# Kernel optimization log

Hardware: AMD Instinct MI355X
Metric: run time of the kernel (lower is better)

Reference implementation:

```python
import jax, jax.numpy as jnp
import numpy as np

B, S, DQ, DK, H, D = 4, 2048, 1024, 1024, 16, 64


def setup_inputs() -> dict:
    key = jax.random.key(0)
    k1, k2, k3, k4 = jax.random.split(key, 4)
    # xavier_uniform bound for Linear(in, out): sqrt(6/(in+out))
    bq = float(np.sqrt(6.0 / (DQ + H * D)))
    bk = float(np.sqrt(6.0 / (DK + H * D)))
    return {
        "query_input": jax.random.normal(k1, (B, S, DQ), dtype=jnp.float32),
        "key_input": jax.random.normal(k2, (B, S, DK), dtype=jnp.float32),
        "Wq": jax.random.uniform(k3, (H * D, DQ), minval=-bq, maxval=bq, dtype=jnp.float32),
        "bq": jnp.zeros((H * D,), dtype=jnp.float32),
        "Wk": jax.random.uniform(k4, (H * D, DK), minval=-bk, maxval=bk, dtype=jnp.float32),
        "bk": jnp.zeros((H * D,), dtype=jnp.float32),
    }


def reference(query_input, key_input, Wq, bq, Wk, bk):
    scaling = D ** (-0.5)
    # projections: (B, S, H*D) -> (B, S, H, D)
    q = (query_input @ Wq.T + bq).reshape(B, S, H, D) * scaling
    k = (key_input @ Wk.T + bk).reshape(B, S, H, D)
    # scores: (B, H, S, S), softmax over keys
    scores = jnp.einsum("bqhd,bkhd->bhqk", q, k)
    attn = jax.nn.softmax(scores, axis=-1)
    # NOTE: module reuses K as the value tensor (no V projection)
    out = jnp.einsum("bhqk,bkhd->bqhd", attn, k)
    return out.reshape(B, S, H * D)
```

## Files before the change

kernel.cpp:

```cpp
#include <hip/hip_runtime.h>
#include <stdint.h>

#define NB 4
#define NS 2048
#define NH 16
#define ND 64
#define NHD 1024
#define NK 1024

typedef __attribute__((ext_vector_type(8))) short short8;
typedef __attribute__((ext_vector_type(4))) float f32x4;
typedef __attribute__((ext_vector_type(16))) float f32x16;
typedef __attribute__((ext_vector_type(4))) unsigned u32x4;

__device__ __forceinline__ unsigned short f2bf(float f) {
    union { float f; unsigned u; } v; v.f = f;
    return (unsigned short)((v.u + 0x7fffu + ((v.u >> 16) & 1u)) >> 16);
}

__device__ __forceinline__ void gload_lds16(const unsigned short* g, unsigned short* l) {
    __builtin_amdgcn_global_load_lds(
        (const __attribute__((address_space(1))) void*)g,
        (__attribute__((address_space(3))) void*)l, 16, 0, 0);
}

__device__ __forceinline__ unsigned cvtpk(float lo, float hi) {
    unsigned r;
    asm volatile("v_cvt_pk_bf16_f32 %0, %1, %2" : "=v"(r) : "v"(lo), "v"(hi));
    return r;
}
__device__ __forceinline__ void plswap(unsigned& a, unsigned& b) {
    asm volatile("v_permlane32_swap_b32 %0, %1" : "+v"(a), "+v"(b));
}
__device__ __forceinline__ float exp2_raw(float x) {
    float r;
    asm("v_exp_f32 %0, %1" : "=v"(r) : "v"(x));
    return r;
}

__global__ void cvt_w_bf16(const float* __restrict__ Wq, const float* __restrict__ Wk,
                           unsigned short* __restrict__ Wqb, unsigned short* __restrict__ Wkb) {
    const int n4 = (NK * NHD) / 4;
    const int stride = gridDim.x * blockDim.x;
    for (int i = blockIdx.x * blockDim.x + threadIdx.x; i < 2 * n4; i += stride) {
        const int m = i < n4 ? 0 : 1;
        const int j = m ? i - n4 : i;
        const float4 v = m ? ((const float4*)Wk)[j] : ((const float4*)Wq)[j];
        ushort4 o;
        o.x = f2bf(v.x); o.y = f2bf(v.y); o.z = f2bf(v.z); o.w = f2bf(v.w);
        if (m) ((ushort4*)Wkb)[j] = o; else ((ushort4*)Wqb)[j] = o;
    }
}


#define RD_AF(KK)                                                                         \
    _Pragma("unroll")                                                                     \
    for (int mi_ = 0; mi_ < 4; ++mi_) {                                                   \
        const int rowA_ = wm + mi_ * 16 + lr;                                             \
        af[mi_] = *(const short8*)(Ab + (rowA_ << 7) + (((KK) * 64 + lg * 16) ^ swzr));   \
    }
#define RD_BF(KK)                                                                         \
    _Pragma("unroll")                                                                     \
    for (int ni_ = 0; ni_ < 4; ++ni_) {                                                   \
        const int rowB_ = wn + ni_ * 16 + lr;                                             \
        bfr[ni_] = *(const short8*)(Bb + (rowB_ << 7) + (((KK) * 64 + lg * 16) ^ swzr));  \
    }
#define DO_MFMA16()                                                                       \
    do {                                                                                  \
        __builtin_amdgcn_s_setprio(1);                                                    \
        _Pragma("unroll")                                                                 \
        for (int mi_ = 0; mi_ < 4; ++mi_)                                                 \
            _Pragma("unroll")                                                             \
            for (int ni_ = 0; ni_ < 4; ++ni_)                                             \
                acc[mi_][ni_] = __builtin_amdgcn_mfma_f32_16x16x32_bf16(                  \
                    af[mi_], bfr[ni_], acc[mi_][ni_], 0, 0, 0);                           \
        __builtin_amdgcn_s_setprio(0);                                                    \
    } while (0)

__global__ __launch_bounds__(256, 2) void proj_gemm7(
    const float* __restrict__ Xq,
    const float* __restrict__ Xk,
    const unsigned short* __restrict__ Wqb,
    const unsigned short* __restrict__ Wkb,
    const float* __restrict__ bqv,
    const float* __restrict__ bkv,
    unsigned short* __restrict__ Qo,
    unsigned short* __restrict__ Ko,
    unsigned short* __restrict__ KTo,
    float qscale)
{
    __shared__ __attribute__((aligned(16))) char smem[65536];

    const int bid = blockIdx.x;
    const int wg = (bid & 7) * 128 + (bid >> 3);
    const int mp = wg >> 3;
    const int nb = wg & 7;
    const int which = mp >> 6;
    const long bm = (long)(mp & 63) * 128;
    const long bn = (long)nb * 128;

    const float* A32         = which ? Xk : Xq;
    const unsigned short* Wt = which ? Wkb : Wqb;
    const float* bias        = which ? bkv : bqv;
    unsigned short* outp     = which ? Ko : Qo;
    unsigned short* outT     = which ? KTo : nullptr;
    const float scale        = which ? 1.0f : qscale;

    const int t = threadIdx.x;
    const int lane = t & 63;
    const int w = t >> 6;
    const int wm = (w >> 1) * 64, wn = (w & 1) * 64;
    const int lr = lane & 15, lg = lane >> 4;
    const int swzr = (lr & 7) << 4;

    f32x4 acc[4][4];
    #pragma unroll
    for (int i = 0; i < 4; ++i)
        #pragma unroll
        for (int jj = 0; jj < 4; ++jj) acc[i][jj] = (f32x4){0.f, 0.f, 0.f, 0.f};

    float4 aset[8];

    auto LOADA = [&](int k0) {
        #pragma unroll
        for (int c = 0; c < 4; ++c) {
            const int u2 = c * 256 + t;
            const int row = u2 >> 3, c8 = u2 & 7;
            const float* src = A32 + (bm + row) * (long)NK + k0 + c8 * 8;
            aset[2 * c]     = *(const float4*)src;
            aset[2 * c + 1] = *(const float4*)(src + 4);
        }
    };
    auto WRITEA = [&](int buf) {
        char* Ad = smem + buf * 16384;
        #pragma unroll
        for (int c = 0; c < 4; ++c) {
            const int u2 = c * 256 + t;
            const int row = u2 >> 3;
            const int cbyte = ((u2 & 7) << 4) ^ ((row & 7) << 4);
            u32x4 wv;
            wv[0] = cvtpk(aset[2 * c].x, aset[2 * c].y);
            wv[1] = cvtpk(aset[2 * c].z, aset[2 * c].w);
            wv[2] = cvtpk(aset[2 * c + 1].x, aset[2 * c + 1].y);
            wv[3] = cvtpk(aset[2 * c + 1].z, aset[2 * c + 1].w);
            *(u32x4*)(Ad + (row << 7) + cbyte) = wv;
        }
    };
    const int scolB = (((lane & 7) ^ (lane >> 3)) << 3);
    auto BGLOAD = [&](int k0, int buf) {
        unsigned short* Bd = (unsigned short*)(smem + 32768 + buf * 16384);
        #pragma unroll
        for (int c = 0; c < 4; ++c) {
            const int rowB = c * 32 + w * 8 + (lane >> 3);
            gload_lds16(Wt + (bn + rowB) * (long)NK + k0 + scolB,
                        Bd + (size_t)(c * 32 + w * 8) * 64);
        }
    };

    BGLOAD(0, 0);
    asm volatile("" ::: "memory");
    LOADA(0);
    asm volatile("" ::: "memory");
    WRITEA(0);
    __builtin_amdgcn_sched_barrier(0);
    LOADA(64);
    asm volatile("s_waitcnt lgkmcnt(0)" ::: "memory");
    __builtin_amdgcn_s_barrier();
    __builtin_amdgcn_sched_barrier(0);

    for (int it = 0; it < 16; ++it) {
        const int cur = it & 1;
        const char* Ab = (const char*)smem + cur * 16384;
        const char* Bb = (const char*)smem + 32768 + cur * 16384;
        short8 af[4], bfr[4];

        if (it + 1 < 16) BGLOAD((it + 1) * 64, cur ^ 1);

        RD_BF(0); RD_AF(0);
        DO_MFMA16();
        if (it + 1 < 16) WRITEA(cur ^ 1);
        RD_BF(1); RD_AF(1);
        if (it + 2 < 16) LOADA((it + 2) * 64);
        DO_MFMA16();

        if (it + 2 < 16) asm volatile("s_waitcnt vmcnt(8)" ::: "memory");
        else             asm volatile("s_waitcnt vmcnt(0)" ::: "memory");
        asm volatile("s_waitcnt lgkmcnt(0)" ::: "memory");
        __builtin_amdgcn_s_barrier();
        __builtin_amdgcn_sched_barrier(0);
    }

    const int h = (int)((bn + wn) >> 6);
    float bvv[4];
    #pragma unroll
    for (int ni = 0; ni < 4; ++ni) bvv[ni] = bias[(int)bn + wn + ni * 16 + lr];
    #pragma unroll
    for (int mi = 0; mi < 4; ++mi) {
        const int m0 = (int)bm + wm + mi * 16 + lg * 4;
        const int b = m0 >> 11, s0 = m0 & 2047;
        unsigned short vv[4][4];
        #pragma unroll
        for (int ni = 0; ni < 4; ++ni)
            #pragma unroll
            for (int r = 0; r < 4; ++r)
                vv[ni][r] = f2bf((acc[mi][ni][r] + bvv[ni]) * scale);
        unsigned short* orow = outp + (((size_t)(b * NH + h)) * NS + s0) * ND;
        #pragma unroll
        for (int r = 0; r < 4; ++r)
            #pragma unroll
            for (int ni = 0; ni < 4; ++ni)
                orow[(size_t)r * ND + ni * 16 + lr] = vv[ni][r];
        if (outT) {
            #pragma unroll
            for (int ni = 0; ni < 4; ++ni) {
                const int d = ni * 16 + lr;
                ushort4 tv; tv.x = vv[ni][0]; tv.y = vv[ni][1]; tv.z = vv[ni][2]; tv.w = vv[ni][3];
                *(ushort4*)&outT[(((size_t)(b * NH + h)) * ND + d) * NS + s0] = tv;
            }
        }
    }
}

#define PACK_P(s0, s1, paw, lsum)                                              \
    do {                                                                       \
        _Pragma("unroll")                                                      \
        for (int tt_ = 0; tt_ < 2; ++tt_) {                                    \
            unsigned c_[8];                                                    \
            _Pragma("unroll")                                                  \
            for (int j_ = 0; j_ < 8; ++j_) {                                   \
                const float plo_ = exp2_raw(tt_ ? s1[2 * j_]     : s0[2 * j_]);   \
                const float phi_ = exp2_raw(tt_ ? s1[2 * j_ + 1] : s0[2 * j_ + 1]); \
                (lsum) += plo_ + phi_;                                         \
                c_[j_] = cvtpk(plo_, phi_);                                    \
            }                                                                  \
            plswap(c_[0], c_[2]); plswap(c_[1], c_[3]);                        \
            plswap(c_[4], c_[6]); plswap(c_[5], c_[7]);                        \
            paw[2 * tt_]     = (u32x4){c_[0], c_[1], c_[2], c_[3]};            \
            paw[2 * tt_ + 1] = (u32x4){c_[4], c_[5], c_[6], c_[7]};            \
        }                                                                      \
    } while (0)

__global__ __launch_bounds__(512, 4) void attn_fused(
    const unsigned short* __restrict__ Qb,
    const unsigned short* __restrict__ Kb,
    const unsigned short* __restrict__ KTb,
    float* __restrict__ outp)
{
    __shared__ __attribute__((aligned(16))) unsigned short LDSA[2 * 4 * 4096];

    const int t = threadIdx.x;
    const int lane = t & 63;
    const int wq = t >> 6;
    const int q5 = lane & 31;
    const int hi = lane >> 5;

    const int Bid = blockIdx.x + 8 * blockIdx.y + 128 * blockIdx.z;
    const int xcd = Bid & 7;
    const int wIdx = Bid >> 3;
    const int qblk = wIdx & 7;
    const int g = xcd * 8 + (wIdx >> 3);
    const int h = g & 15, b = g >> 4;
    const int qbase = qblk * 256 + wq * 32;

    const unsigned short* Qh  = Qb  + ((size_t)(b * NH + h)) * NS * ND;
    const unsigned short* Kh  = Kb  + ((size_t)(b * NH + h)) * NS * ND;
    const unsigned short* KTh = KTb + ((size_t)(b * NH + h)) * ND * NS;

    short8 qB[4];
    {
        const unsigned short* Qrow = Qh + (size_t)(qbase + q5) * ND;
        #pragma unroll
        for (int kd = 0; kd < 4; ++kd)
            qB[kd] = *(const short8*)&Qrow[kd * 16 + hi * 8];
    }

    const int srow = wq * 8 + (lane >> 3);
    const int scol = ((((lane & 7) << 4) ^ ((srow & 7) << 4)) >> 1);

    f32x16 acc0, acc1;
    float l_run = 0.f;
    #pragma unroll
    for (int r = 0; r < 16; ++r) { acc0[r] = 0.f; acc1[r] = 0.f; }

    const int swz = (q5 & 7) << 4;
    const int ro0 = q5 * 128, ro1 = ro0 + 4096;

    auto STAGE = [&](int buf, int kt ) {
        unsigned short* Bd = &LDSA[buf * 16384];
        gload_lds16(Kh  + (size_t)(kt + srow) * ND + scol,        Bd         + wq * 512);
        gload_lds16(KTh + (size_t)srow * NS + kt + scol,          Bd + 4096  + wq * 512);
        gload_lds16(Kh  + (size_t)(kt + 64 + srow) * ND + scol,   Bd + 8192  + wq * 512);
        gload_lds16(KTh + (size_t)srow * NS + (kt + 64) + scol,   Bd + 12288 + wq * 512);
    };

    auto COMPUTE = [&](const char* Kbuf) {
        const char* Ktbuf = Kbuf + 8192;

        f32x16 s0, s1;
        #pragma unroll
        for (int r = 0; r < 16; ++r) { s0[r] = 0.f; s1[r] = 0.f; }
        __builtin_amdgcn_s_setprio(1);
        #pragma unroll
        for (int kd = 0; kd < 4; ++kd) {
            const int cb = (kd * 32 + hi * 16) ^ swz;
            short8 kf0 = *(const short8*)(Kbuf + ro0 + cb);
            short8 kf1 = *(const short8*)(Kbuf + ro1 + cb);
            s0 = __builtin_amdgcn_mfma_f32_32x32x16_bf16(kf0, qB[kd], s0, 0, 0, 0);
            s1 = __builtin_amdgcn_mfma_f32_32x32x16_bf16(kf1, qB[kd], s1, 0, 0, 0);
        }
        __builtin_amdgcn_s_setprio(0);

        u32x4 paw[4];
        PACK_P(s0, s1, paw, l_run);

        __builtin_amdgcn_s_setprio(1);
        #pragma unroll
        for (int ks = 0; ks < 4; ++ks) {
            union { u32x4 u; short8 s; } pa; pa.u = paw[ks];
            const int cb = (ks * 32 + hi * 16) ^ swz;
            short8 vf0 = *(const short8*)(Ktbuf + ro0 + cb);
            short8 vf1 = *(const short8*)(Ktbuf + ro1 + cb);
            acc0 = __builtin_amdgcn_mfma_f32_32x32x16_bf16(pa.s, vf0, acc0, 0, 0, 0);
            acc1 = __builtin_amdgcn_mfma_f32_32x32x16_bf16(pa.s, vf1, acc1, 0, 0, 0);
        }
        __builtin_amdgcn_s_setprio(0);
    };

    STAGE(0, 0);
    for (int it = 0; it < NS / 128; ++it) {
        const int cur = it & 1;
        asm volatile("s_waitcnt vmcnt(0)" ::: "memory");
        __syncthreads();
        if (it < NS / 128 - 1) STAGE(cur ^ 1, (it + 1) * 128);

        const char* base = (const char*)LDSA + cur * 32768;
        COMPUTE(base);
        COMPUTE(base + 16384);
    }

    const float lt = l_run + __shfl_xor(l_run, 32);
    const float inv = 1.0f / lt;
    #pragma unroll
    for (int r = 0; r < 16; ++r) {
        const int qr = (r & 3) + 8 * (r >> 2) + 4 * hi;
        const float invr = __shfl(inv, qr);
        float* orow = outp + ((size_t)b * NS + (qbase + qr)) * NHD + h * ND;
        orow[q5]      = acc0[r] * invr;
        orow[32 + q5] = acc1[r] * invr;
    }
}

extern "C" void kernel_launch(void* const* d_in, const int* in_sizes, int n_in,
                              void* d_out, int out_size, void* d_ws, size_t ws_size,
                              hipStream_t stream) {
    const float* xq = (const float*)d_in[0];
    const float* xk = (const float*)d_in[1];
    const float* Wq = (const float*)d_in[2];
    const float* bq = (const float*)d_in[3];
    const float* Wk = (const float*)d_in[4];
    const float* bk = (const float*)d_in[5];
    float* outp = (float*)d_out;

    unsigned short* Wqb = (unsigned short*)d_ws;
    unsigned short* Wkb = Wqb + 1048576;
    unsigned short* Qb  = Wkb + 1048576;
    unsigned short* Kb  = Qb  + 8388608;
    unsigned short* KTb = Kb  + 8388608;

    cvt_w_bf16<<<1024, 256, 0, stream>>>(Wq, Wk, Wqb, Wkb);

    const float qscale = 0.125f * 1.4426950408889634f;
    proj_gemm7<<<1024, 256, 0, stream>>>(xq, xk, Wqb, Wkb, bq, bk,
                                         Qb, Kb, KTb, qscale);

    attn_fused<<<dim3(8, 16, 4), 512, 0, stream>>>(Qb, Kb, KTb, outp);
}
```

Baseline: 141.3 us.

## Enlarge projection GEMM tiles to 256x256 with 1024-thread blocks

The projection GEMM moves from 128x128 tiles with 256 threads and 64KB static LDS to 256x256 tiles with 1024 threads (16 waves) and 128KB dynamic LDS. The A and B load mappings, the wait counts and the grid size are adjusted to match. Larger tiles raise data reuse per byte loaded from global memory. In exchange only one workgroup fits per CU because of LDS, and only 256 blocks are launched, which limits latency hiding and may leave CUs underused.

```diff
diff --git a/kernel.cpp b/kernel.cpp
--- a/kernel.cpp
+++ b/kernel.cpp
@@ -77,7 +77,7 @@
         __builtin_amdgcn_s_setprio(0);                                                    \
     } while (0)
 
-__global__ __launch_bounds__(256, 2) void proj_gemm7(
+__global__ __launch_bounds__(1024, 4) void proj_gemm8(
     const float* __restrict__ Xq,
     const float* __restrict__ Xk,
     const unsigned short* __restrict__ Wqb,
@@ -89,15 +89,15 @@
     unsigned short* __restrict__ KTo,
     float qscale)
 {
-    __shared__ __attribute__((aligned(16))) char smem[65536];
+    extern __shared__ __attribute__((aligned(16))) char smem[];
 
     const int bid = blockIdx.x;
-    const int wg = (bid & 7) * 128 + (bid >> 3);
-    const int mp = wg >> 3;
-    const int nb = wg & 7;
-    const int which = mp >> 6;
-    const long bm = (long)(mp & 63) * 128;
-    const long bn = (long)nb * 128;
+    const int wg = (bid & 7) * 32 + (bid >> 3);
+    const int mp = wg >> 2;
+    const int nb = wg & 3;
+    const int which = mp >> 5;
+    const long bm = (long)(mp & 31) * 256;
+    const long bn = (long)nb * 256;
 
     const float* A32         = which ? Xk : Xq;
     const unsigned short* Wt = which ? Wkb : Wqb;
@@ -109,7 +109,7 @@
     const int t = threadIdx.x;
     const int lane = t & 63;
     const int w = t >> 6;
-    const int wm = (w >> 1) * 64, wn = (w & 1) * 64;
+    const int wm = (w >> 2) * 64, wn = (w & 3) * 64;
     const int lr = lane & 15, lg = lane >> 4;
     const int swzr = (lr & 7) << 4;
 
@@ -119,41 +119,36 @@
         #pragma unroll
         for (int jj = 0; jj < 4; ++jj) acc[i][jj] = (f32x4){0.f, 0.f, 0.f, 0.f};
 
-    float4 aset[8];
+    float4 aset[4];
 
     auto LOADA = [&](int k0) {
-        #pragma unroll
-        for (int c = 0; c < 4; ++c) {
-            const int u2 = c * 256 + t;
-            const int row = u2 >> 3, c8 = u2 & 7;
-            const float* src = A32 + (bm + row) * (long)NK + k0 + c8 * 8;
-            aset[2 * c]     = *(const float4*)src;
-            aset[2 * c + 1] = *(const float4*)(src + 4);
-        }
+        const float* src = A32 + (bm + (t >> 2)) * (long)NK + k0 + (t & 3) * 16;
+        #pragma unroll
+        for (int j = 0; j < 4; ++j) aset[j] = ((const float4*)src)[j];
     };
     auto WRITEA = [&](int buf) {
-        char* Ad = smem + buf * 16384;
-        #pragma unroll
-        for (int c = 0; c < 4; ++c) {
-            const int u2 = c * 256 + t;
-            const int row = u2 >> 3;
-            const int cbyte = ((u2 & 7) << 4) ^ ((row & 7) << 4);
+        char* Ad = smem + buf * 32768;
+        const int row = t >> 2;
+        #pragma unroll
+        for (int h2 = 0; h2 < 2; ++h2) {
+            const int slot = (t & 3) * 2 + h2;
+            const int cbyte = (slot << 4) ^ ((row & 7) << 4);
             u32x4 wv;
-            wv[0] = cvtpk(aset[2 * c].x, aset[2 * c].y);
-            wv[1] = cvtpk(aset[2 * c].z, aset[2 * c].w);
-            wv[2] = cvtpk(aset[2 * c + 1].x, aset[2 * c + 1].y);
-            wv[3] = cvtpk(aset[2 * c + 1].z, aset[2 * c + 1].w);
+            wv[0] = cvtpk(aset[2 * h2].x, aset[2 * h2].y);
+            wv[1] = cvtpk(aset[2 * h2].z, aset[2 * h2].w);
+            wv[2] = cvtpk(aset[2 * h2 + 1].x, aset[2 * h2 + 1].y);
+            wv[3] = cvtpk(aset[2 * h2 + 1].z, aset[2 * h2 + 1].w);
             *(u32x4*)(Ad + (row << 7) + cbyte) = wv;
         }
     };
     const int scolB = (((lane & 7) ^ (lane >> 3)) << 3);
     auto BGLOAD = [&](int k0, int buf) {
-        unsigned short* Bd = (unsigned short*)(smem + 32768 + buf * 16384);
-        #pragma unroll
-        for (int c = 0; c < 4; ++c) {
-            const int rowB = c * 32 + w * 8 + (lane >> 3);
+        unsigned short* Bd = (unsigned short*)(smem + 65536 + buf * 32768);
+        #pragma unroll
+        for (int c = 0; c < 2; ++c) {
+            const int rowB = c * 128 + w * 8 + (lane >> 3);
             gload_lds16(Wt + (bn + rowB) * (long)NK + k0 + scolB,
-                        Bd + (size_t)(c * 32 + w * 8) * 64);
+                        Bd + (size_t)(c * 128 + w * 8) * 64);
         }
     };
 
@@ -170,8 +165,8 @@
 
     for (int it = 0; it < 16; ++it) {
         const int cur = it & 1;
-        const char* Ab = (const char*)smem + cur * 16384;
-        const char* Bb = (const char*)smem + 32768 + cur * 16384;
+        const char* Ab = (const char*)smem + cur * 32768;
+        const char* Bb = (const char*)smem + 65536 + cur * 32768;
         short8 af[4], bfr[4];
 
         if (it + 1 < 16) BGLOAD((it + 1) * 64, cur ^ 1);
@@ -183,7 +178,7 @@
         if (it + 2 < 16) LOADA((it + 2) * 64);
         DO_MFMA16();
 
-        if (it + 2 < 16) asm volatile("s_waitcnt vmcnt(8)" ::: "memory");
+        if (it + 2 < 16) asm volatile("s_waitcnt vmcnt(4)" ::: "memory");
         else             asm volatile("s_waitcnt vmcnt(0)" ::: "memory");
         asm volatile("s_waitcnt lgkmcnt(0)" ::: "memory");
         __builtin_amdgcn_s_barrier();
@@ -367,11 +362,18 @@
     unsigned short* Kb  = Qb  + 8388608;
     unsigned short* KTb = Kb  + 8388608;
 
+    static bool lds_init = false;
+    if (!lds_init) {
+        hipFuncSetAttribute((const void*)proj_gemm8,
+                            hipFuncAttributeMaxDynamicSharedMemorySize, 131072);
+        lds_init = true;
+    }
+
     cvt_w_bf16<<<1024, 256, 0, stream>>>(Wq, Wk, Wqb, Wkb);
 
     const float qscale = 0.125f * 1.4426950408889634f;
-    proj_gemm7<<<1024, 256, 0, stream>>>(xq, xk, Wqb, Wkb, bq, bk,
-                                         Qb, Kb, KTb, qscale);
+    proj_gemm8<<<256, 1024, 131072, stream>>>(xq, xk, Wqb, Wkb, bq, bk,
+                                              Qb, Kb, KTb, qscale);
 
     attn_fused<<<dim3(8, 16, 4), 512, 0, stream>>>(Qb, Kb, KTb, outp);
 }
```

Result: faster. 134.2 us (-5.0%).
